# Kernel tuning notes

Hardware: AMD Instinct MI355X
Metric: run time of the kernel (lower is better)

## Reference

```python
import jax, jax.numpy as jnp
import numpy as np

B, N, D, E = 8, 96, 512, 4
ALPHA = 0.2  # LeakyReLU negative slope (init arg `alpha`)


def setup_inputs() -> dict:
    key = jax.random.key(0)
    ks = jax.random.split(key, 12)
    nodes = jax.random.normal(ks[0], (B, N, D), jnp.float32)
    # edges[0]: in-edge type weights, edges[1]: out-edge type weights, each [E, D, D]
    edges = jax.random.normal(ks[1], (2, E, D, D), jnp.float32) * 0.05
    adj_in_type = jax.random.randint(ks[2], (B, N, N), 0, E)
    adj_out_type = jax.random.randint(ks[3], (B, N, N), 0, E)
    eye = jnp.eye(N, dtype=bool)  # self-loop guarantees no all-masked softmax row
    exist_in = (jax.random.uniform(ks[4], (B, N, N)) < 0.1) | eye
    exist_out = (jax.random.uniform(ks[5], (B, N, N)) < 0.1) | eye
    Wa_in = jax.random.normal(ks[6], (2 * D, 1), jnp.float32) * 0.02
    ba_in = jnp.zeros((1,), jnp.float32)
    Wa_out = jax.random.normal(ks[7], (2 * D, 1), jnp.float32) * 0.02
    ba_out = jnp.zeros((1,), jnp.float32)
    Wr = jax.random.normal(ks[8], (3 * D, D), jnp.float32) * 0.02
    br = jnp.zeros((D,), jnp.float32)
    Wz = jax.random.normal(ks[9], (3 * D, D), jnp.float32) * 0.02
    bz = jnp.zeros((D,), jnp.float32)
    Wh = jax.random.normal(ks[10], (3 * D, D), jnp.float32) * 0.02
    bh = jnp.zeros((D,), jnp.float32)
    return dict(nodes=nodes, edges=edges, adj_in_type=adj_in_type, adj_out_type=adj_out_type,
                exist_in=exist_in, exist_out=exist_out, Wa_in=Wa_in, ba_in=ba_in,
                Wa_out=Wa_out, ba_out=ba_out, Wr=Wr, br=br, Wz=Wz, bz=bz, Wh=Wh, bh=bh)


def _edge_messages(nodes, W_types, adj_type, exist):
    """msgs[b,i,j] = nodes[b,j] @ W_types[adj_type[b,i,j]] if edge (i<-j) exists else 0.
    Vectorizes the original triple Python loop: transform all nodes by all E edge
    types once, then gather per (b,i,j). nodes [B,N,D], W_types [E,D,D]."""
    all_msgs = jnp.einsum('bjh,ehd->bejd', nodes, W_types)  # [B,E,N,D]
    b_idx = jnp.arange(nodes.shape[0])[:, None, None]
    j_idx = jnp.arange(nodes.shape[1])[None, None, :]
    msgs = all_msgs[b_idx, adj_type, j_idx]                 # [B,N,N,D]
    return jnp.where(exist[..., None], msgs, 0.0)


def _graph_attention(node_h, msgs, exist, Wa, ba):
    """GAT over the N neighbor slots of each node (softmax along last N axis).
    node_h [B,N,D] is broadcast to pairs, matching node_hidden.unsqueeze(2).repeat."""
    h_rep = jnp.broadcast_to(node_h[:, :, None, :], msgs.shape)  # [B,N,N,D]
    feat = jnp.concatenate([h_rep, msgs], axis=-1)               # [B,N,N,2D]
    score = jax.nn.leaky_relu((feat @ Wa)[..., 0] + ba[0], ALPHA)  # [B,N,N]
    score = jnp.where(exist, score, -1e9)
    attn = jax.nn.softmax(score, axis=-1)
    return jnp.einsum('bij,bijd->bid', attn, msgs)               # [B,N,D]


def reference(nodes, edges, adj_in_type, adj_out_type, exist_in, exist_out,
              Wa_in, ba_in, Wa_out, ba_out, Wr, br, Wz, bz, Wh, bh):
    msgs_in = _edge_messages(nodes, edges[0], adj_in_type, exist_in)
    msgs_out = _edge_messages(nodes, edges[1], adj_out_type, exist_out)
    in_h = _graph_attention(nodes, msgs_in, exist_in, Wa_in, ba_in)
    out_h = _graph_attention(nodes, msgs_out, exist_out, Wa_out, ba_out)
    # Propagator: GGNN-style gated fusion of nodes with in/out aggregates
    a = jnp.concatenate([in_h, out_h], axis=-1)      # [B,N,2D]
    az = jnp.concatenate([a, nodes], axis=-1)        # [B,N,3D]
    r = jax.nn.sigmoid(az @ Wr + br)
    z = jax.nn.sigmoid(az @ Wz + bz)
    h_hat = jnp.tanh(jnp.concatenate([a, r * nodes], axis=-1) @ Wh + bh)
    return (1.0 - z) * nodes + z * h_hat
```

## Files before the change

kernel.cpp:

```cpp
#include <hip/hip_runtime.h>
#include <hip/hip_bf16.h>

#define BB 8
#define NN 96
#define DD 512
#define EE 4
#define ROWS 768

typedef __attribute__((ext_vector_type(8))) short s8v;
typedef __attribute__((ext_vector_type(4))) short s4v;
typedef __attribute__((ext_vector_type(4))) float f32x4;

#define WS_PROJP   4096
#define WS_NODESH  1048576
#define WS_ALLMSGS 2097152
#define WS_ACAT    8388608
#define WS_EDGEST  10747904
#define WS_WT      14942208
#define WS_RN      19660800
#define WS_ZB      20447232
#define WS_HPRE    22020096

__device__ __forceinline__ short f2bf(float x) {
  unsigned int u = __builtin_bit_cast(unsigned int, x);
  u += 0x7FFFu + ((u >> 16) & 1u);
  return (short)(u >> 16);
}
__device__ __forceinline__ float b2f(short s) {
  unsigned int u = ((unsigned int)(unsigned short)s) << 16;
  return __builtin_bit_cast(float, u);
}

__device__ __forceinline__ f32x4 mfma16(s8v a, s8v b, f32x4 c) {
  asm("v_mfma_f32_16x16x32_bf16 %0, %1, %2, %0" : "+v"(c) : "v"(a), "v"(b));
  return c;
}

__device__ __forceinline__ int get_exist(const void* p, int code, int idx) {
  switch (code) {
    case 0: return ((const unsigned char*)p)[idx] != 0;
    case 1: return ((const int*)p)[idx] != 0;
    case 2: return ((const float*)p)[idx] != 0.0f;
    default: return ((const long long*)p)[idx] != 0;
  }
}

__global__ __launch_bounds__(256) void k_prep(const float* __restrict__ edges,
                                              const float* __restrict__ Wr,
                                              const float* __restrict__ Wz,
                                              const float* __restrict__ Wh,
                                              const float* __restrict__ nodes,
                                              const void* exist_in,
                                              const void* exist_out,
                                              short* __restrict__ edgesT,
                                              short* __restrict__ WT,
                                              short* __restrict__ nodesH,
                                              short* __restrict__ AcatH,
                                              int* __restrict__ flags) {
  __shared__ float t[64][65];
  __shared__ int red[3];
  int task = blockIdx.x;
  int tt = threadIdx.x;
  if (task < 1088) {
    const float* src;
    short* dst;
    int dstPitch, r0, c0;
    if (task < 512) {
      int e = task >> 6, rem = task & 63;
      src = edges + (size_t)e * DD * DD;
      dst = edgesT + (size_t)e * DD * DD;
      dstPitch = DD;
      r0 = (rem >> 3) * 64; c0 = (rem & 7) * 64;
    } else {
      int q = task - 512;
      int z = q / 192, rem = q % 192;
      src = z == 0 ? Wr : (z == 1 ? Wz : Wh);
      dst = WT + (size_t)z * (512 * 1536);
      dstPitch = 1536;
      r0 = (rem >> 3) * 64; c0 = (rem & 7) * 64;
    }
    int row = tt >> 2, c16 = (tt & 3) * 16;
    const float* sp = src + (size_t)(r0 + row) * DD + c0 + c16;
#pragma unroll
    for (int i = 0; i < 4; ++i) {
      float4 v = *(const float4*)(sp + i * 4);
      t[row][c16 + i * 4 + 0] = v.x; t[row][c16 + i * 4 + 1] = v.y;
      t[row][c16 + i * 4 + 2] = v.z; t[row][c16 + i * 4 + 3] = v.w;
    }
    __syncthreads();
    short* dp = dst + (size_t)(c0 + row) * dstPitch + r0 + c16;
#pragma unroll
    for (int i = 0; i < 4; ++i) {
      s4v o;
      o[0] = f2bf(t[c16 + i * 4 + 0][row]);
      o[1] = f2bf(t[c16 + i * 4 + 1][row]);
      o[2] = f2bf(t[c16 + i * 4 + 2][row]);
      o[3] = f2bf(t[c16 + i * 4 + 3][row]);
      *(s4v*)(dp + i * 4) = o;
    }
  } else if (task < 1100) {
    int r0 = (task - 1088) * 64;
    int c4 = (tt & 127) * 4;
#pragma unroll 4
    for (int p2 = 0; p2 < 32; ++p2) {
      int row = r0 + p2 * 2 + (tt >> 7);
      float4 v = *(const float4*)(nodes + (size_t)row * DD + c4);
      s4v o;
      o[0] = f2bf(v.x); o[1] = f2bf(v.y); o[2] = f2bf(v.z); o[3] = f2bf(v.w);
      *(s4v*)(nodesH + (size_t)row * DD + c4) = o;
      *(s4v*)(AcatH + (size_t)row * 1536 + 1024 + c4) = o;
    }
  } else {
    int y = task - 1100;
    if (tt < 3) red[tt] = 0;
    __syncthreads();
    const uint4* p = (const uint4*)(y ? exist_out : exist_in);
    int mis = 0, gt = 0, od = 0;
    for (int i = tt; i < 4608; i += 256) {
      uint4 v = p[i];
      unsigned any = v.x | v.y | v.z | v.w;
      if (any) {
        if (any & 0xFFFFFF00u) mis = 1;
        if (any & 0xFEFEFEFEu) gt = 1;
        if (v.y | v.w) od = 1;
      }
    }
    if (mis) atomicOr(&red[0], 1);
    if (gt) atomicOr(&red[1], 1);
    if (od) atomicOr(&red[2], 1);
    __syncthreads();
    if (tt == 0) flags[y] = red[0] ? (red[1] ? 2 : 0) : (red[2] ? 1 : 3);
  }
}

__device__ __forceinline__ void mfma_tile(const short* As, const short* Bs,
                                          int wr, int wc, int l, f32x4 acc[2][2]) {
  int lr = l & 15, lg = l >> 4;
#pragma unroll
  for (int ks = 0; ks < 64; ks += 32) {
    s8v a0 = *(const s8v*)&As[(wr + lr) * 72 + ks + 8 * lg];
    s8v a1 = *(const s8v*)&As[(wr + 16 + lr) * 72 + ks + 8 * lg];
    s8v b0 = *(const s8v*)&Bs[(wc + lr) * 72 + ks + 8 * lg];
    s8v b1 = *(const s8v*)&Bs[(wc + 16 + lr) * 72 + ks + 8 * lg];
    acc[0][0] = mfma16(a0, b0, acc[0][0]);
    acc[0][1] = mfma16(a0, b1, acc[0][1]);
    acc[1][0] = mfma16(a1, b0, acc[1][0]);
    acc[1][1] = mfma16(a1, b1, acc[1][1]);
  }
}

__global__ __launch_bounds__(256) void k_gemm_msgs(const short* __restrict__ nodesH,
                                                   const short* __restrict__ edgesT,
                                                   const float* __restrict__ Wa_in,
                                                   const float* __restrict__ Wa_out,
                                                   short* __restrict__ C,
                                                   float* __restrict__ projp) {
  __shared__ __align__(16) short As[64 * 72];
  __shared__ __align__(16) short Bs[64 * 72];
  __shared__ float pp[128];
  int tid = threadIdx.x;
  int row0 = blockIdx.y * 64;
  int col0 = blockIdx.x * 64;
  int de = col0 >> 9, h0 = col0 & 511;
  int w = tid >> 6, l = tid & 63;
  int wr = (w >> 1) * 32, wc = (w & 1) * 32;
  int srow = tid >> 2, scc = (tid & 3) * 16;
  const short* Ap = nodesH + (size_t)(row0 + srow) * DD + scc;
  const short* Bp = edgesT + (size_t)de * DD * DD + (size_t)(h0 + srow) * DD + scc;
  s8v a0 = *(const s8v*)Ap, a1 = *(const s8v*)(Ap + 8);
  s8v b0 = *(const s8v*)Bp, b1 = *(const s8v*)(Bp + 8);
  f32x4 acc[2][2] = {};
  for (int k0 = 0; k0 < DD; k0 += 64) {
    *(s8v*)&As[srow * 72 + scc] = a0; *(s8v*)&As[srow * 72 + scc + 8] = a1;
    *(s8v*)&Bs[srow * 72 + scc] = b0; *(s8v*)&Bs[srow * 72 + scc + 8] = b1;
    __syncthreads();
    if (k0 + 64 < DD) {
      Ap += 64; Bp += 64;
      a0 = *(const s8v*)Ap; a1 = *(const s8v*)(Ap + 8);
      b0 = *(const s8v*)Bp; b1 = *(const s8v*)(Bp + 8);
    }
    mfma_tile(As, Bs, wr, wc, l, acc);
    __syncthreads();
  }
  asm volatile("s_nop 7\n\ts_nop 7");
  int lr = l & 15, lg4 = (l >> 4) * 4;
#pragma unroll
  for (int fi = 0; fi < 2; ++fi)
#pragma unroll
    for (int fj = 0; fj < 2; ++fj) {
      f32x4 v = acc[fi][fj];
#pragma unroll
      for (int r = 0; r < 4; ++r) {
        int row = row0 + wr + fi * 16 + lg4 + r;
        int col = h0 + wc + fj * 16 + lr;
        C[((size_t)(de * ROWS + row)) * DD + col] = f2bf(v[r]);
      }
    }
  const float* wa2 = ((de >> 2) ? Wa_out : Wa_in) + DD;
  float w0 = wa2[h0 + wc + lr];
  float w1 = wa2[h0 + wc + 16 + lr];
  float pr[2][4];
#pragma unroll
  for (int fi = 0; fi < 2; ++fi)
#pragma unroll
    for (int r = 0; r < 4; ++r)
      pr[fi][r] = acc[fi][0][r] * w0 + acc[fi][1][r] * w1;
#pragma unroll
  for (int off = 1; off < 16; off <<= 1)
#pragma unroll
    for (int fi = 0; fi < 2; ++fi)
#pragma unroll
      for (int r = 0; r < 4; ++r) pr[fi][r] += __shfl_xor(pr[fi][r], off);
  if (lr == 0) {
#pragma unroll
    for (int fi = 0; fi < 2; ++fi)
#pragma unroll
      for (int r = 0; r < 4; ++r)
        pp[(w & 1) * 64 + wr + fi * 16 + lg4 + r] = pr[fi][r];
  }
  __syncthreads();
  if (tid < 64)
    projp[(size_t)(blockIdx.x & 7) * 6144 + de * ROWS + row0 + tid] =
        pp[tid] + pp[64 + tid];
}

__global__ __launch_bounds__(256) void k_attn(const short* __restrict__ allmsgsH,
                                              const float* __restrict__ projp,
                                              const int* __restrict__ adj_in,
                                              const int* __restrict__ adj_out,
                                              const void* exist_in,
                                              const void* exist_out,
                                              const int* __restrict__ fr,
                                              const float* __restrict__ nodes,
                                              const float* __restrict__ Wa_in,
                                              const float* __restrict__ ba_in,
                                              const float* __restrict__ Wa_out,
                                              const float* __restrict__ ba_out,
                                              short* __restrict__ AcatH) {
  __shared__ float s_w[NN];
  __shared__ int s_off[NN];
  __shared__ int s_list[NN];
  __shared__ int s_cnt[2];
  __shared__ float s_part[5];
  int blk = blockIdx.x;
  int dir = blk / ROWS;
  int row = blk % ROWS;
  int b = row / NN;
  const int* adj = dir ? adj_out : adj_in;
  const void* ex = dir ? exist_out : exist_in;
  int code = fr[dir];
  int t = threadIdx.x, wv = t >> 6, lane = t & 63;
  const float* wa = dir ? Wa_out : Wa_in;
  float2 nv = *(const float2*)(nodes + (size_t)row * DD + 2 * t);
  float p = fmaf(nv.x, wa[2 * t], nv.y * wa[2 * t + 1]);
#pragma unroll
  for (int off = 32; off; off >>= 1) p += __shfl_xor(p, off);
  if (lane == 0) s_part[wv] = p;
  int ex_ = 0, tj_ = 0;
  if (t < NN) {
    int idx = row * NN + t;
    ex_ = get_exist(ex, code, idx);
    tj_ = adj[idx];
    s_off[t] = ((dir * 4 + tj_) * ROWS + b * NN + t) * DD;
  }
  if (wv == 0) {
    unsigned long long m = __ballot(ex_);
    int pos = __popcll(m & ((1ull << lane) - 1));
    if (ex_) s_list[pos] = t;
    if (lane == 0) s_cnt[0] = (int)__popcll(m);
  } else if (wv == 1) {
    unsigned long long m = __ballot(t < NN && ex_);
    int pos = __popcll(m & ((1ull << lane) - 1));
    if (t < NN && ex_) s_list[64 + pos] = t;
    if (lane == 0) s_cnt[1] = (int)__popcll(m);
  }
  __syncthreads();
  float s1v = s_part[0] + s_part[1] + s_part[2] + s_part[3] +
              (dir ? ba_out[0] : ba_in[0]);
  if (t < NN) {
    float sc = -1e9f;
    if (ex_) {
      size_t base = (size_t)(dir * 4 + tj_) * ROWS + b * NN + t;
      float pv = 0.f;
#pragma unroll
      for (int c = 0; c < 8; ++c) pv += projp[(size_t)c * 6144 + base];
      float x = s1v + pv;
      sc = x >= 0.f ? x : 0.2f * x;
    }
    s_w[t] = sc;
  }
  __syncthreads();
  if (t < 64) {
    float e1 = s_w[t];
    float e2 = (t < 32) ? s_w[t + 64] : -1e30f;
    float mx = fmaxf(e1, e2);
#pragma unroll
    for (int off = 32; off; off >>= 1) mx = fmaxf(mx, __shfl_xor(mx, off));
    float w1 = (e1 > -1e8f) ? __expf(e1 - mx) : 0.f;
    float w2 = (t < 32 && e2 > -1e8f) ? __expf(e2 - mx) : 0.f;
    s_w[t] = w1;
    if (t < 32) s_w[t + 64] = w2;
    float sm = w1 + w2;
#pragma unroll
    for (int off = 32; off; off >>= 1) sm += __shfl_xor(sm, off);
    if (t == 0) s_part[4] = 1.f / sm;
  }
  __syncthreads();
  float inv = s_part[4];
  int c0 = s_cnt[0], c1 = s_cnt[1];
  float acc0 = 0.f, acc1 = 0.f;
  int t2 = 2 * t;
#pragma unroll 4
  for (int q = 0; q < c0; ++q) {
    int j = s_list[q];
    float wj = s_w[j];
    unsigned u = *(const unsigned*)(allmsgsH + s_off[j] + t2);
    acc0 = fmaf(wj, b2f((short)(u & 0xFFFF)), acc0);
    acc1 = fmaf(wj, b2f((short)(u >> 16)), acc1);
  }
#pragma unroll 4
  for (int q = 0; q < c1; ++q) {
    int j = s_list[64 + q];
    float wj = s_w[j];
    unsigned u = *(const unsigned*)(allmsgsH + s_off[j] + t2);
    acc0 = fmaf(wj, b2f((short)(u & 0xFFFF)), acc0);
    acc1 = fmaf(wj, b2f((short)(u >> 16)), acc1);
  }
  unsigned o0 = (unsigned short)f2bf(acc0 * inv);
  unsigned o1 = (unsigned short)f2bf(acc1 * inv);
  *(unsigned*)(AcatH + (size_t)row * 1536 + dir * DD + t2) = o0 | (o1 << 16);
}

__global__ __launch_bounds__(256) void k_gemm1(const short* __restrict__ AcatH,
                                               const short* __restrict__ WT,
                                               const float* __restrict__ br,
                                               const float* __restrict__ bz,
                                               const float* __restrict__ nodes,
                                               short* __restrict__ rnH,
                                               float* __restrict__ zb,
                                               float* __restrict__ Hpre) {
  __shared__ __align__(16) short As[64 * 72];
  __shared__ __align__(16) short Bs[64 * 72];
  int tid = threadIdx.x;
  int row0 = blockIdx.y * 64;
  int col0 = blockIdx.x * 64;
  int region = col0 >> 9, c0 = col0 & 511;
  int K = (region == 2) ? 1024 : 1536;
  int w = tid >> 6, l = tid & 63;
  int wr = (w >> 1) * 32, wc = (w & 1) * 32;
  int srow = tid >> 2, scc = (tid & 3) * 16;
  const short* Ap = AcatH + (size_t)(row0 + srow) * 1536 + scc;
  const short* Bp = WT + (size_t)region * (512 * 1536) + (size_t)(c0 + srow) * 1536 + scc;
  s8v a0 = *(const s8v*)Ap, a1 = *(const s8v*)(Ap + 8);
  s8v b0 = *(const s8v*)Bp, b1 = *(const s8v*)(Bp + 8);
  f32x4 acc[2][2] = {};
  for (int k0 = 0; k0 < K; k0 += 64) {
    *(s8v*)&As[srow * 72 + scc] = a0; *(s8v*)&As[srow * 72 + scc + 8] = a1;
    *(s8v*)&Bs[srow * 72 + scc] = b0; *(s8v*)&Bs[srow * 72 + scc + 8] = b1;
    __syncthreads();
    if (k0 + 64 < K) {
      Ap += 64; Bp += 64;
      a0 = *(const s8v*)Ap; a1 = *(const s8v*)(Ap + 8);
      b0 = *(const s8v*)Bp; b1 = *(const s8v*)(Bp + 8);
    }
    mfma_tile(As, Bs, wr, wc, l, acc);
    __syncthreads();
  }
  asm volatile("s_nop 7\n\ts_nop 7");
  int lr = l & 15, lg4 = (l >> 4) * 4;
#pragma unroll
  for (int fi = 0; fi < 2; ++fi)
#pragma unroll
    for (int fj = 0; fj < 2; ++fj) {
      f32x4 v = acc[fi][fj];
#pragma unroll
      for (int r = 0; r < 4; ++r) {
        int row = row0 + wr + fi * 16 + lg4 + r;
        int c = c0 + wc + fj * 16 + lr;
        float vv = v[r];
        size_t o = (size_t)row * DD + c;
        if (region == 0) {
          float s = 1.f / (1.f + __expf(-(vv + br[c])));
          rnH[o] = f2bf(s * nodes[o]);
        } else if (region == 1) {
          zb[o] = 1.f / (1.f + __expf(-(vv + bz[c])));
        } else {
          Hpre[o] = vv;
        }
      }
    }
}

__global__ __launch_bounds__(256) void k_gemm2(const short* __restrict__ rnH,
                                               const short* __restrict__ WT,
                                               const float* __restrict__ bh,
                                               const float* __restrict__ Hpre,
                                               const float* __restrict__ zb,
                                               const float* __restrict__ nodes,
                                               float* __restrict__ out) {
  __shared__ __align__(16) short As[64 * 72];
  __shared__ __align__(16) short Bs[64 * 72];
  int tid = threadIdx.x;
  int row0 = blockIdx.y * 64;
  int col0 = blockIdx.x * 64;
  int w = tid >> 6, l = tid & 63;
  int wr = (w >> 1) * 32, wc = (w & 1) * 32;
  int srow = tid >> 2, scc = (tid & 3) * 16;
  const short* Ap = rnH + (size_t)(row0 + srow) * DD + scc;
  const short* Bp = WT + (size_t)2 * (512 * 1536) + (size_t)(col0 + srow) * 1536 + 1024 + scc;
  s8v a0 = *(const s8v*)Ap, a1 = *(const s8v*)(Ap + 8);
  s8v b0 = *(const s8v*)Bp, b1 = *(const s8v*)(Bp + 8);
  f32x4 acc[2][2] = {};
  for (int k0 = 0; k0 < DD; k0 += 64) {
    *(s8v*)&As[srow * 72 + scc] = a0; *(s8v*)&As[srow * 72 + scc + 8] = a1;
    *(s8v*)&Bs[srow * 72 + scc] = b0; *(s8v*)&Bs[srow * 72 + scc + 8] = b1;
    __syncthreads();
    if (k0 + 64 < DD) {
      Ap += 64; Bp += 64;
      a0 = *(const s8v*)Ap; a1 = *(const s8v*)(Ap + 8);
      b0 = *(const s8v*)Bp; b1 = *(const s8v*)(Bp + 8);
    }
    mfma_tile(As, Bs, wr, wc, l, acc);
    __syncthreads();
  }
  asm volatile("s_nop 7\n\ts_nop 7");
  int lr = l & 15, lg4 = (l >> 4) * 4;
#pragma unroll
  for (int fi = 0; fi < 2; ++fi)
#pragma unroll
    for (int fj = 0; fj < 2; ++fj) {
      f32x4 v = acc[fi][fj];
#pragma unroll
      for (int r = 0; r < 4; ++r) {
        int row = row0 + wr + fi * 16 + lg4 + r;
        int c = col0 + wc + fj * 16 + lr;
        size_t o = (size_t)row * DD + c;
        float h = tanhf(v[r] + Hpre[o] + bh[c]);
        float zz = zb[o];
        float nd = nodes[o];
        out[o] = (1.f - zz) * nd + zz * h;
      }
    }
}

extern "C" void kernel_launch(void* const* d_in, const int* in_sizes, int n_in,
                              void* d_out, int out_size, void* d_ws, size_t ws_size,
                              hipStream_t stream) {
  const float* nodes = (const float*)d_in[0];
  const float* edges = (const float*)d_in[1];
  const int* adj_in = (const int*)d_in[2];
  const int* adj_out = (const int*)d_in[3];
  const void* exist_in = d_in[4];
  const void* exist_out = d_in[5];
  const float* Wa_in = (const float*)d_in[6];
  const float* ba_in = (const float*)d_in[7];
  const float* Wa_out = (const float*)d_in[8];
  const float* ba_out = (const float*)d_in[9];
  const float* Wr = (const float*)d_in[10];
  const float* br = (const float*)d_in[11];
  const float* Wz = (const float*)d_in[12];
  const float* bz = (const float*)d_in[13];
  const float* Wh = (const float*)d_in[14];
  const float* bh = (const float*)d_in[15];

  char* ws = (char*)d_ws;
  int* flags = (int*)ws;
  float* projp = (float*)(ws + WS_PROJP);
  short* nodesH = (short*)(ws + WS_NODESH);
  short* allmsgsH = (short*)(ws + WS_ALLMSGS);
  short* AcatH = (short*)(ws + WS_ACAT);
  short* edgesT = (short*)(ws + WS_EDGEST);
  short* WT = (short*)(ws + WS_WT);
  short* rnH = (short*)(ws + WS_RN);
  float* zb = (float*)(ws + WS_ZB);
  float* Hpre = (float*)(ws + WS_HPRE);
  float* out = (float*)d_out;

  k_prep<<<1102, 256, 0, stream>>>(edges, Wr, Wz, Wh, nodes, exist_in,
                                   exist_out, edgesT, WT, nodesH, AcatH, flags);
  k_gemm_msgs<<<dim3(64, 12), 256, 0, stream>>>(nodesH, edgesT, Wa_in, Wa_out,
                                                allmsgsH, projp);
  k_attn<<<2 * ROWS, 256, 0, stream>>>(allmsgsH, projp, adj_in, adj_out,
                                       exist_in, exist_out, flags, nodes,
                                       Wa_in, ba_in, Wa_out, ba_out, AcatH);
  k_gemm1<<<dim3(24, 12), 256, 0, stream>>>(AcatH, WT, br, bz, nodes, rnH, zb,
                                            Hpre);
  k_gemm2<<<dim3(8, 12), 256, 0, stream>>>(rnH, WT, bh, Hpre, zb, nodes, out);
}
```

Baseline: 61.37 us.

## Move gate-weight transposes into attention kernel to shorten prep critical path

The Wr/Wz/Wh fp32-to-bf16 transposes move out of the prep kernel and run as extra 576 blocks appended to the attention kernel grid. Their only consumer is the later gate GEMM, so prep now finishes sooner and the message GEMM can start earlier. The transpose work then shares the GPU with the attention blocks. The nodes-conversion task is also split into more, smaller blocks (48×16 rows instead of 12×64). The cost is that every attention block now reserves a 64×65 float shared-memory tile, which may lower attention occupancy.

```diff
diff --git a/kernel.cpp b/kernel.cpp
--- a/kernel.cpp
+++ b/kernel.cpp
@@ -45,15 +45,35 @@
   }
 }
 
+__device__ __forceinline__ void tr64(const float* __restrict__ src,
+                                     short* __restrict__ dst, int dstPitch,
+                                     int r0, int c0, float (*t)[65], int tt) {
+  int row = tt >> 2, c16 = (tt & 3) * 16;
+  const float* sp = src + (size_t)(r0 + row) * DD + c0 + c16;
+#pragma unroll
+  for (int i = 0; i < 4; ++i) {
+    float4 v = *(const float4*)(sp + i * 4);
+    t[row][c16 + i * 4 + 0] = v.x; t[row][c16 + i * 4 + 1] = v.y;
+    t[row][c16 + i * 4 + 2] = v.z; t[row][c16 + i * 4 + 3] = v.w;
+  }
+  __syncthreads();
+  short* dp = dst + (size_t)(c0 + row) * dstPitch + r0 + c16;
+#pragma unroll
+  for (int i = 0; i < 4; ++i) {
+    s4v o;
+    o[0] = f2bf(t[c16 + i * 4 + 0][row]);
+    o[1] = f2bf(t[c16 + i * 4 + 1][row]);
+    o[2] = f2bf(t[c16 + i * 4 + 2][row]);
+    o[3] = f2bf(t[c16 + i * 4 + 3][row]);
+    *(s4v*)(dp + i * 4) = o;
+  }
+}
+
 __global__ __launch_bounds__(256) void k_prep(const float* __restrict__ edges,
-                                              const float* __restrict__ Wr,
-                                              const float* __restrict__ Wz,
-                                              const float* __restrict__ Wh,
                                               const float* __restrict__ nodes,
                                               const void* exist_in,
                                               const void* exist_out,
                                               short* __restrict__ edgesT,
-                                              short* __restrict__ WT,
                                               short* __restrict__ nodesH,
                                               short* __restrict__ AcatH,
                                               int* __restrict__ flags) {
@@ -61,48 +81,15 @@
   __shared__ int red[3];
   int task = blockIdx.x;
   int tt = threadIdx.x;
-  if (task < 1088) {
-    const float* src;
-    short* dst;
-    int dstPitch, r0, c0;
-    if (task < 512) {
-      int e = task >> 6, rem = task & 63;
-      src = edges + (size_t)e * DD * DD;
-      dst = edgesT + (size_t)e * DD * DD;
-      dstPitch = DD;
-      r0 = (rem >> 3) * 64; c0 = (rem & 7) * 64;
-    } else {
-      int q = task - 512;
-      int z = q / 192, rem = q % 192;
-      src = z == 0 ? Wr : (z == 1 ? Wz : Wh);
-      dst = WT + (size_t)z * (512 * 1536);
-      dstPitch = 1536;
-      r0 = (rem >> 3) * 64; c0 = (rem & 7) * 64;
-    }
-    int row = tt >> 2, c16 = (tt & 3) * 16;
-    const float* sp = src + (size_t)(r0 + row) * DD + c0 + c16;
-#pragma unroll
-    for (int i = 0; i < 4; ++i) {
-      float4 v = *(const float4*)(sp + i * 4);
-      t[row][c16 + i * 4 + 0] = v.x; t[row][c16 + i * 4 + 1] = v.y;
-      t[row][c16 + i * 4 + 2] = v.z; t[row][c16 + i * 4 + 3] = v.w;
-    }
-    __syncthreads();
-    short* dp = dst + (size_t)(c0 + row) * dstPitch + r0 + c16;
-#pragma unroll
-    for (int i = 0; i < 4; ++i) {
-      s4v o;
-      o[0] = f2bf(t[c16 + i * 4 + 0][row]);
-      o[1] = f2bf(t[c16 + i * 4 + 1][row]);
-      o[2] = f2bf(t[c16 + i * 4 + 2][row]);
-      o[3] = f2bf(t[c16 + i * 4 + 3][row]);
-      *(s4v*)(dp + i * 4) = o;
-    }
-  } else if (task < 1100) {
-    int r0 = (task - 1088) * 64;
+  if (task < 512) {
+    int e = task >> 6, rem = task & 63;
+    tr64(edges + (size_t)e * DD * DD, edgesT + (size_t)e * DD * DD, DD,
+         (rem >> 3) * 64, (rem & 7) * 64, t, tt);
+  } else if (task < 560) {
+    int r0 = (task - 512) * 16;
     int c4 = (tt & 127) * 4;
-#pragma unroll 4
-    for (int p2 = 0; p2 < 32; ++p2) {
+#pragma unroll
+    for (int p2 = 0; p2 < 8; ++p2) {
       int row = r0 + p2 * 2 + (tt >> 7);
       float4 v = *(const float4*)(nodes + (size_t)row * DD + c4);
       s4v o;
@@ -111,7 +98,7 @@
       *(s4v*)(AcatH + (size_t)row * 1536 + 1024 + c4) = o;
     }
   } else {
-    int y = task - 1100;
+    int y = task - 560;
     if (tt < 3) red[tt] = 0;
     __syncthreads();
     const uint4* p = (const uint4*)(y ? exist_out : exist_in);
@@ -236,20 +223,34 @@
                                               const float* __restrict__ ba_in,
                                               const float* __restrict__ Wa_out,
                                               const float* __restrict__ ba_out,
+                                              const float* __restrict__ Wr,
+                                              const float* __restrict__ Wz,
+                                              const float* __restrict__ Wh,
+                                              short* __restrict__ WT,
                                               short* __restrict__ AcatH) {
+  __shared__ float trb[64][65];
   __shared__ float s_w[NN];
   __shared__ int s_off[NN];
   __shared__ int s_list[NN];
   __shared__ int s_cnt[2];
   __shared__ float s_part[5];
   int blk = blockIdx.x;
+  int t = threadIdx.x;
+  if (blk >= 1536) {
+    int q = blk - 1536;
+    int z = q / 192, rem = q % 192;
+    const float* src = z == 0 ? Wr : (z == 1 ? Wz : Wh);
+    tr64(src, WT + (size_t)z * (512 * 1536), 1536, (rem >> 3) * 64,
+         (rem & 7) * 64, trb, t);
+    return;
+  }
   int dir = blk / ROWS;
   int row = blk % ROWS;
   int b = row / NN;
   const int* adj = dir ? adj_out : adj_in;
   const void* ex = dir ? exist_out : exist_in;
   int code = fr[dir];
-  int t = threadIdx.x, wv = t >> 6, lane = t & 63;
+  int wv = t >> 6, lane = t & 63;
   const float* wa = dir ? Wa_out : Wa_in;
   float2 nv = *(const float2*)(nodes + (size_t)row * DD + 2 * t);
   float p = fmaf(nv.x, wa[2 * t], nv.y * wa[2 * t + 1]);
@@ -476,13 +477,14 @@
   float* Hpre = (float*)(ws + WS_HPRE);
   float* out = (float*)d_out;
 
-  k_prep<<<1102, 256, 0, stream>>>(edges, Wr, Wz, Wh, nodes, exist_in,
-                                   exist_out, edgesT, WT, nodesH, AcatH, flags);
+  k_prep<<<562, 256, 0, stream>>>(edges, nodes, exist_in, exist_out, edgesT,
+                                  nodesH, AcatH, flags);
   k_gemm_msgs<<<dim3(64, 12), 256, 0, stream>>>(nodesH, edgesT, Wa_in, Wa_out,
                                                 allmsgsH, projp);
-  k_attn<<<2 * ROWS, 256, 0, stream>>>(allmsgsH, projp, adj_in, adj_out,
-                                       exist_in, exist_out, flags, nodes,
-                                       Wa_in, ba_in, Wa_out, ba_out, AcatH);
+  k_attn<<<1536 + 576, 256, 0, stream>>>(allmsgsH, projp, adj_in, adj_out,
+                                         exist_in, exist_out, flags, nodes,
+                                         Wa_in, ba_in, Wa_out, ba_out, Wr, Wz,
+                                         Wh, WT, AcatH);
   k_gemm1<<<dim3(24, 12), 256, 0, stream>>>(AcatH, WT, br, bz, nodes, rnH, zb,
                                             Hpre);
   k_gemm2<<<dim3(8, 12), 256, 0, stream>>>(rnH, WT, bh, Hpre, zb, nodes, out);
```

Result: no change. 60.42 us, median of 2 (-1.5%).
